# Optimization experiments

Hardware: AMD Instinct MI355X
Metric: run time of the kernel (lower is better)

The kernel has to match this reference:

```python
import jax, jax.numpy as jnp
import numpy as np

N_NODES = 50000
N_EDGES = 800000
N_GRAPHS = 256
IN_DIM = 128
HID = 64
HEADS = 4
N_CLASSES = 2
NEG_SLOPE = 0.2


def gat_conv(h, W, attn_l, attn_r, bias, src, dst, n_heads, out_dim):
    """DGL-style GATConv. h: [N, Fin] -> [N, H, D]."""
    n = h.shape[0]
    feat = (h @ W).reshape(n, n_heads, out_dim)            # [N,H,D]
    el = jnp.sum(feat * attn_l, axis=-1)                   # [N,H]
    er = jnp.sum(feat * attn_r, axis=-1)                   # [N,H]
    e = jax.nn.leaky_relu(el[src] + er[dst], NEG_SLOPE)    # [E,H]
    # edge softmax over incoming edges of each dst node (numerically stable)
    emax = jax.ops.segment_max(e, dst, num_segments=n)     # [N,H]
    emax = jnp.where(jnp.isfinite(emax), emax, 0.0)
    ee = jnp.exp(e - emax[dst])                            # [E,H]
    denom = jax.ops.segment_sum(ee, dst, num_segments=n)   # [N,H]
    alpha = ee / jnp.maximum(denom, 1e-9)[dst]             # [E,H]
    msg = alpha[:, :, None] * feat[src]                    # [E,H,D]
    rst = jax.ops.segment_sum(msg, dst, num_segments=n)    # [N,H,D]
    return rst + bias.reshape(1, n_heads, out_dim)


def setup_inputs() -> dict:
    key = jax.random.key(0)
    ks = jax.random.split(key, 16)
    h = jax.random.normal(ks[0], (N_NODES, IN_DIM), dtype=jnp.float32)
    src = jax.random.randint(ks[1], (N_EDGES,), 0, N_NODES, dtype=jnp.int32)
    dst = jax.random.randint(ks[2], (N_EDGES,), 0, N_NODES, dtype=jnp.int32)
    graph_ids = jnp.sort(jax.random.randint(ks[3], (N_NODES,), 0, N_GRAPHS, dtype=jnp.int32))
    s1 = 1.0 / np.sqrt(IN_DIM)
    s2 = 1.0 / np.sqrt(HID * HEADS)
    sc = 1.0 / np.sqrt(HID)
    W1 = jax.random.normal(ks[4], (IN_DIM, HEADS * HID), dtype=jnp.float32) * s1
    attn_l1 = jax.random.normal(ks[5], (HEADS, HID), dtype=jnp.float32) * sc
    attn_r1 = jax.random.normal(ks[6], (HEADS, HID), dtype=jnp.float32) * sc
    b1 = jnp.zeros((HEADS * HID,), dtype=jnp.float32)
    W2 = jax.random.normal(ks[7], (HEADS * HID, 1 * HID), dtype=jnp.float32) * s2
    attn_l2 = jax.random.normal(ks[8], (1, HID), dtype=jnp.float32) * sc
    attn_r2 = jax.random.normal(ks[9], (1, HID), dtype=jnp.float32) * sc
    b2 = jnp.zeros((HID,), dtype=jnp.float32)
    Wc = jax.random.normal(ks[10], (HID, N_CLASSES), dtype=jnp.float32) * sc
    bc = jnp.zeros((N_CLASSES,), dtype=jnp.float32)
    return {"h": h, "src": src, "dst": dst, "graph_ids": graph_ids,
            "W1": W1, "attn_l1": attn_l1, "attn_r1": attn_r1, "b1": b1,
            "W2": W2, "attn_l2": attn_l2, "attn_r2": attn_r2, "b2": b2,
            "Wc": Wc, "bc": bc}


def reference(h, src, dst, graph_ids, W1, attn_l1, attn_r1, b1,
              W2, attn_l2, attn_r2, b2, Wc, bc):
    # layer 1: [N, IN] -> [N, HEADS, HID] -> relu -> flatten heads
    x = jax.nn.relu(gat_conv(h, W1, attn_l1, attn_r1, b1, src, dst, HEADS, HID))
    x = x.reshape(N_NODES, HEADS * HID)
    # layer 2: single head -> [N, HID]
    x = jax.nn.relu(gat_conv(x, W2, attn_l2, attn_r2, b2, src, dst, 1, HID))
    x = x.reshape(N_NODES, HID)
    # dropout p=0.3 is identity at eval time
    # AvgPooling: mean of node features per graph
    sums = jax.ops.segment_sum(x, graph_ids, num_segments=N_GRAPHS)      # [G,HID]
    cnts = jax.ops.segment_sum(jnp.ones((N_NODES,), x.dtype), graph_ids,
                               num_segments=N_GRAPHS)                    # [G]
    pooled = sums / jnp.maximum(cnts, 1.0)[:, None]
    return pooled @ Wc + bc                                              # [G, n_classes]
```

## Files before the change

kernel.cpp:

```cpp
#include <hip/hip_runtime.h>
#include <math.h>

#define NN 50000
#define NE 800000
#define NG 256
#define IND 128
#define NBUCK 98
#define CHUNK 4096
#define NPBLK ((NE + CHUNK - 1) / CHUNK)

typedef __bf16 bf16_t;
typedef bf16_t bf16x8 __attribute__((ext_vector_type(8)));
typedef float f32x4 __attribute__((ext_vector_type(4)));
typedef float floatx2 __attribute__((ext_vector_type(2)));
typedef unsigned short ushortx8 __attribute__((ext_vector_type(8)));

__device__ __forceinline__ float lrelu(float x) { return fmaxf(x, 0.2f * x); }
__device__ __forceinline__ float b2f(unsigned short u) {
  return __uint_as_float(((unsigned)u) << 16);
}
__device__ __forceinline__ float blo(unsigned u) { return __uint_as_float(u << 16); }
__device__ __forceinline__ float bhi(unsigned u) { return __uint_as_float(u & 0xffff0000u); }
__device__ __forceinline__ unsigned short f2b(float f) {
  unsigned u = __float_as_uint(f);
  return (unsigned short)((u + 0x7fffu + ((u >> 16) & 1u)) >> 16);
}
__device__ __forceinline__ float sel4(float v0, float v1, float v2, float v3, int g) {
  float a01 = (g & 1) ? v1 : v0;
  float a23 = (g & 1) ? v3 : v2;
  return (g & 2) ? a23 : a01;
}

__global__ __launch_bounds__(1024) void k_zero(int* __restrict__ counts) {
  int i = blockIdx.x * 1024 + threadIdx.x;
  if (i < NN) counts[i] = 0;
}

__global__ __launch_bounds__(256) void k_prep(const float* __restrict__ W1,
                                              const int* __restrict__ dst,
                                              unsigned short* __restrict__ w1t_hi,
                                              int* __restrict__ counts) {
  int tid = blockIdx.x * 256 + threadIdx.x;
  if (tid < 256 * IND) {
    int c = tid >> 7, k = tid & 127;
    w1t_hi[tid] = f2b(W1[(size_t)k * 256 + c]);
  }
  if (tid < NE) atomicAdd(&counts[dst[tid]], 1);
}

__global__ __launch_bounds__(256) void k_gemm1(const float* __restrict__ h,
                                               const unsigned short* __restrict__ w1t_hi,
                                               const float* __restrict__ al,
                                               const float* __restrict__ ar,
                                               unsigned int* __restrict__ feat1f8,
                                               float4* __restrict__ el1,
                                               float4* __restrict__ er1) {
  __shared__ unsigned short w1s[256 * IND];
  int t = threadIdx.x;
  for (int i = t; i < 4096; i += 256) {
    int c = i >> 4, k8 = i & 15;
    ushortx8 v = ((const ushortx8*)w1t_hi)[i];
    int byte = (c * 256 + k8 * 16) ^ ((c & 7) << 4);
    *(ushortx8*)((char*)w1s + byte) = v;
  }
  __syncthreads();
  int w = t >> 6, l = t & 63;
  int c0 = l & 15, kg = l >> 4;
  int rw = blockIdx.x * 64 + w * 16;
  int arow = rw + c0;
  if (arow >= NN) arow = NN - 1;
  const float4* hp = (const float4*)h + (size_t)arow * 32 + kg * 2;
  f32x4 acc[16] = {};
#pragma unroll
  for (int ks = 0; ks < 4; ks++) {
    float4 v0 = hp[ks * 8], v1 = hp[ks * 8 + 1];
    float f[8] = {v0.x, v0.y, v0.z, v0.w, v1.x, v1.y, v1.z, v1.w};
    ushortx8 uh, ul;
#pragma unroll
    for (int j = 0; j < 8; j++) {
      unsigned short hj = f2b(f[j]);
      uh[j] = hj;
      ul[j] = f2b(f[j] - b2f(hj));
    }
    bf16x8 ah = *(bf16x8*)&uh;
    bf16x8 alo = *(bf16x8*)&ul;
#pragma unroll
    for (int n = 0; n < 16; n++) {
      int col = n * 16 + c0;
      int byte = (col * 256 + (ks * 4 + kg) * 16) ^ ((col & 7) << 4);
      bf16x8 b = *(const bf16x8*)(const void*)((const char*)w1s + byte);
      acc[n] = __builtin_amdgcn_mfma_f32_16x16x32_bf16(alo, b, acc[n], 0, 0, 0);
      acc[n] = __builtin_amdgcn_mfma_f32_16x16x32_bf16(ah, b, acc[n], 0, 0, 0);
    }
  }
  float alv[16], arv[16];
#pragma unroll
  for (int n = 0; n < 16; n++) {
    int ai = (n >> 2) * 64 + (n & 3) * 16 + c0;
    alv[n] = al[ai];
    arv[n] = ar[ai];
  }
#pragma unroll
  for (int j = 0; j < 4; j++) {
    int node = rw + kg * 4 + j;
    bool ok = node < NN;
    float pl[4] = {0.f, 0.f, 0.f, 0.f}, pr[4] = {0.f, 0.f, 0.f, 0.f};
#pragma unroll
    for (int dq = 0; dq < 4; dq++) {
      float v0 = acc[dq][j], v1 = acc[4 | dq][j], v2 = acc[8 | dq][j], v3 = acc[12 | dq][j];
      if (ok) {
        int u = __builtin_amdgcn_cvt_pk_fp8_f32(v0, v1, 0, false);
        u = __builtin_amdgcn_cvt_pk_fp8_f32(v2, v3, u, true);
        feat1f8[(size_t)node * 64 + dq * 16 + c0] = (unsigned)u;
      }
    }
#pragma unroll
    for (int n = 0; n < 16; n++) {
      float cv = acc[n][j];
      int hh = n >> 2;
      pl[hh] += cv * alv[n];
      pr[hh] += cv * arv[n];
    }
#pragma unroll
    for (int off = 1; off < 16; off <<= 1) {
#pragma unroll
      for (int hh = 0; hh < 4; hh++) {
        pl[hh] += __shfl_xor(pl[hh], off);
        pr[hh] += __shfl_xor(pr[hh], off);
      }
    }
    if (c0 == 0 && ok) {
      el1[node] = make_float4(pl[0], pl[1], pl[2], pl[3]);
      er1[node] = make_float4(pr[0], pr[1], pr[2], pr[3]);
    }
  }
}

#define NSB ((NN + 1023) / 1024)
__global__ __launch_bounds__(1024) void k_scanA(const int* __restrict__ counts,
                                                int* __restrict__ bsums) {
  int gid = blockIdx.x * 1024 + threadIdx.x;
  int v = (gid < NN) ? counts[gid] : 0;
#pragma unroll
  for (int off = 32; off; off >>= 1) v += __shfl_xor(v, off);
  __shared__ int ws[16];
  int w = threadIdx.x >> 6, l = threadIdx.x & 63;
  if (l == 0) ws[w] = v;
  __syncthreads();
  if (threadIdx.x == 0) {
    int s = 0;
#pragma unroll
    for (int i = 0; i < 16; i++) s += ws[i];
    bsums[blockIdx.x] = s;
  }
}

__global__ __launch_bounds__(64) void k_scanB(const int* __restrict__ bsums,
                                              int* __restrict__ boffs,
                                              int* __restrict__ bcursor) {
  int l = threadIdx.x;
  int orig = (l < NSB) ? bsums[l] : 0;
  int v = orig;
#pragma unroll
  for (int off = 1; off < 64; off <<= 1) {
    int tv = __shfl_up(v, off);
    if (l >= off) v += tv;
  }
  if (l < NSB) boffs[l] = v - orig;
  for (int i = l; i < NBUCK; i += 64) bcursor[i] = 0;
}

__global__ __launch_bounds__(1024) void k_scanC(const int* __restrict__ counts,
                                                const int* __restrict__ boffs,
                                                int* __restrict__ offs) {
  int gid = blockIdx.x * 1024 + threadIdx.x;
  int orig = (gid < NN) ? counts[gid] : 0;
  int v = orig;
  int w = threadIdx.x >> 6, l = threadIdx.x & 63;
#pragma unroll
  for (int off = 1; off < 64; off <<= 1) {
    int tv = __shfl_up(v, off);
    if (l >= off) v += tv;
  }
  __shared__ int ws[16];
  if (l == 63) ws[w] = v;
  __syncthreads();
  int woff = 0;
#pragma unroll
  for (int i = 0; i < 16; i++)
    if (i < w) woff += ws[i];
  if (gid < NN) offs[gid] = boffs[blockIdx.x] + woff + v - orig;
  if (gid == 0) offs[NN] = NE;
}

__global__ __launch_bounds__(256) void k_part(const int* __restrict__ src, const int* __restrict__ dst,
                                              const int* __restrict__ offs, int* __restrict__ bcursor,
                                              int2* __restrict__ ebuf) {
  __shared__ int lcnt[NBUCK];
  __shared__ int lbase[NBUCK];
  __shared__ int gb[NBUCK];
  int t = threadIdx.x;
  for (int i = t; i < NBUCK; i += 256) lcnt[i] = 0;
  __syncthreads();
  int e0 = blockIdx.x * CHUNK;
  int sv[16], dv[16], rk[16];
#pragma unroll
  for (int i = 0; i < 16; i++) {
    int e = e0 + i * 256 + t;
    if (e < NE) {
      sv[i] = src[e];
      dv[i] = dst[e];
      rk[i] = atomicAdd(&lcnt[dv[i] >> 9], 1);
    }
  }
  __syncthreads();
  for (int i = t; i < NBUCK; i += 256) {
    lbase[i] = atomicAdd(&bcursor[i], lcnt[i]);
    gb[i] = offs[i << 9];
  }
  __syncthreads();
#pragma unroll
  for (int i = 0; i < 16; i++) {
    int e = e0 + i * 256 + t;
    if (e < NE) {
      int b = dv[i] >> 9;
      int2 v;
      v.x = sv[i];
      v.y = dv[i];
      ebuf[gb[b] + lbase[b] + rk[i]] = v;
    }
  }
}

__global__ __launch_bounds__(256) void k_scat2(const int2* __restrict__ ebuf, const int* __restrict__ offs,
                                               int2* __restrict__ sd) {
  __shared__ int lcur[512];
  int b = blockIdx.x, t = threadIdx.x;
  for (int i = t; i < 512; i += 256) lcur[i] = 0;
  int n0 = b << 9;
  int n1 = n0 + 512;
  if (n1 > NN) n1 = NN;
  int lo = offs[n0], hi = offs[n1];
  __syncthreads();
  for (int i = lo + t; i < hi; i += 256) {
    int2 p = ebuf[i];
    int pos = atomicAdd(&lcur[p.y - n0], 1);
    sd[offs[p.y] + pos] = p;
  }
}

__global__ __launch_bounds__(256) void k_edge1(const int2* __restrict__ sd,
                                               const float4* __restrict__ el1,
                                               const float4* __restrict__ er1,
                                               int4* __restrict__ erec1) {
  int i = blockIdx.x * 256 + threadIdx.x;
  if (i >= NE) return;
  int2 p = sd[i];
  float4 l = el1[p.x], r = er1[p.y];
  unsigned w0 = f2b(__expf(lrelu(l.x + r.x)));
  unsigned w1 = f2b(__expf(lrelu(l.y + r.y)));
  unsigned w2 = f2b(__expf(lrelu(l.z + r.z)));
  unsigned w3 = f2b(__expf(lrelu(l.w + r.w)));
  int4 o;
  o.x = p.x;
  o.y = (int)(w0 | (w1 << 16));
  o.z = (int)(w2 | (w3 << 16));
  o.w = 0;
  erec1[i] = o;
}

__global__ __launch_bounds__(256) void k_agg1(const int* __restrict__ offs, const int4* __restrict__ erec1,
                                              const unsigned int* __restrict__ feat1f8,
                                              const float* __restrict__ b1,
                                              unsigned short* __restrict__ x1b) {
  int wid = (blockIdx.x * 256 + threadIdx.x) >> 6;
  int lane = threadIdx.x & 63;
  if (wid >= NN) return;
  int g = lane >> 4, q = lane & 15;
  int start = offs[wid], end = offs[wid + 1];
  float a[4][4] = {};
  float ds0 = 0.f, ds1 = 0.f, ds2 = 0.f, ds3 = 0.f;
  int i = start;
  for (; i + 8 <= end; i += 8) {
    int4 r0 = erec1[i + g];
    int4 r1 = erec1[i + 4 + g];
    uint4 u0 = *(const uint4*)(feat1f8 + (size_t)r0.x * 64 + q * 4);
    uint4 u1 = *(const uint4*)(feat1f8 + (size_t)r1.x * 64 + q * 4);
    float w00 = blo((unsigned)r0.y), w01 = bhi((unsigned)r0.y);
    float w02 = blo((unsigned)r0.z), w03 = bhi((unsigned)r0.z);
    float w10 = blo((unsigned)r1.y), w11 = bhi((unsigned)r1.y);
    float w12 = blo((unsigned)r1.z), w13 = bhi((unsigned)r1.z);
#pragma unroll
    for (int dj = 0; dj < 4; dj++) {
      unsigned ua = (&u0.x)[dj], ub = (&u1.x)[dj];
      floatx2 lo0 = __builtin_amdgcn_cvt_pk_f32_fp8(ua, false);
      floatx2 hi0 = __builtin_amdgcn_cvt_pk_f32_fp8(ua, true);
      floatx2 lo1 = __builtin_amdgcn_cvt_pk_f32_fp8(ub, false);
      floatx2 hi1 = __builtin_amdgcn_cvt_pk_f32_fp8(ub, true);
      a[dj][0] += w00 * lo0[0] + w10 * lo1[0];
      a[dj][1] += w01 * lo0[1] + w11 * lo1[1];
      a[dj][2] += w02 * hi0[0] + w12 * hi1[0];
      a[dj][3] += w03 * hi0[1] + w13 * hi1[1];
    }
    ds0 += w00 + w10; ds1 += w01 + w11; ds2 += w02 + w12; ds3 += w03 + w13;
  }
  for (; i < end; i += 4) {
    int e = i + g;
    bool valid = e < end;
    int ec = valid ? e : end - 1;
    int4 r0 = erec1[ec];
    float w00 = blo((unsigned)r0.y), w01 = bhi((unsigned)r0.y);
    float w02 = blo((unsigned)r0.z), w03 = bhi((unsigned)r0.z);
    if (!valid) { w00 = 0.f; w01 = 0.f; w02 = 0.f; w03 = 0.f; }
    uint4 u0 = *(const uint4*)(feat1f8 + (size_t)r0.x * 64 + q * 4);
#pragma unroll
    for (int dj = 0; dj < 4; dj++) {
      unsigned ua = (&u0.x)[dj];
      floatx2 lo0 = __builtin_amdgcn_cvt_pk_f32_fp8(ua, false);
      floatx2 hi0 = __builtin_amdgcn_cvt_pk_f32_fp8(ua, true);
      a[dj][0] += w00 * lo0[0];
      a[dj][1] += w01 * lo0[1];
      a[dj][2] += w02 * hi0[0];
      a[dj][3] += w03 * hi0[1];
    }
    ds0 += w00; ds1 += w01; ds2 += w02; ds3 += w03;
  }
#pragma unroll
  for (int off = 16; off < 64; off <<= 1) {
#pragma unroll
    for (int dj = 0; dj < 4; dj++) {
#pragma unroll
      for (int hh = 0; hh < 4; hh++) a[dj][hh] += __shfl_xor(a[dj][hh], off);
    }
    ds0 += __shfl_xor(ds0, off);
    ds1 += __shfl_xor(ds1, off);
    ds2 += __shfl_xor(ds2, off);
    ds3 += __shfl_xor(ds3, off);
  }
  float dsg = sel4(ds0, ds1, ds2, ds3, g);
  float inv = 1.f / fmaxf(dsg, 1e-9f);
  float4 bb = *(const float4*)(b1 + g * 64 + q * 4);
  ushort4 ov;
  ov.x = f2b(fmaxf(sel4(a[0][0], a[0][1], a[0][2], a[0][3], g) * inv + bb.x, 0.f));
  ov.y = f2b(fmaxf(sel4(a[1][0], a[1][1], a[1][2], a[1][3], g) * inv + bb.y, 0.f));
  ov.z = f2b(fmaxf(sel4(a[2][0], a[2][1], a[2][2], a[2][3], g) * inv + bb.z, 0.f));
  ov.w = f2b(fmaxf(sel4(a[3][0], a[3][1], a[3][2], a[3][3], g) * inv + bb.w, 0.f));
  *(ushort4*)(x1b + (size_t)wid * 256 + g * 64 + q * 4) = ov;
}

__global__ __launch_bounds__(256) void k_gemm2(const unsigned short* __restrict__ x1b,
                                               const float* __restrict__ W2,
                                               const float* __restrict__ al2,
                                               const float* __restrict__ ar2,
                                               unsigned int* __restrict__ feat2f8,
                                               float* __restrict__ el2,
                                               float* __restrict__ er2) {
  __shared__ unsigned short w2t[64 * 256];
  int t = threadIdx.x;
  for (int i = t; i < 64 * 256; i += 256) {
    int k = i >> 6, col = i & 63;
    int kg = k >> 3;
    int s = (col * 32 + kg) ^ (col & 7);
    w2t[s * 8 + (k & 7)] = f2b(W2[i]);
  }
  __syncthreads();
  int w = t >> 6, l = t & 63;
  int rw = blockIdx.x * 64 + w * 16;
  int arow = rw + (l & 15);
  if (arow >= NN) arow = NN - 1;
  const unsigned short* aptr = x1b + (size_t)arow * 256 + (l >> 4) * 8;
  f32x4 acc[4] = {};
#pragma unroll
  for (int ks = 0; ks < 8; ks++) {
    bf16x8 a = *(const bf16x8*)(const void*)(aptr + ks * 32);
#pragma unroll
    for (int n = 0; n < 4; n++) {
      int colg = n * 16 + (l & 15);
      int kg = ks * 4 + (l >> 4);
      int s = (colg * 32 + kg) ^ (colg & 7);
      bf16x8 b = *(const bf16x8*)(const void*)&w2t[s * 8];
      acc[n] = __builtin_amdgcn_mfma_f32_16x16x32_bf16(a, b, acc[n], 0, 0, 0);
    }
  }
  float al2v[4], ar2v[4];
#pragma unroll
  for (int n = 0; n < 4; n++) { al2v[n] = al2[n * 16 + (l & 15)]; ar2v[n] = ar2[n * 16 + (l & 15)]; }
#pragma unroll
  for (int j = 0; j < 4; j++) {
    int node = rw + (l >> 4) * 4 + j;
    float pl = 0.f, pr = 0.f;
    float c0v = acc[0][j], c1v = acc[1][j], c2v = acc[2][j], c3v = acc[3][j];
    if (node < NN) {
      int u = __builtin_amdgcn_cvt_pk_fp8_f32(c0v, c1v, 0, false);
      u = __builtin_amdgcn_cvt_pk_fp8_f32(c2v, c3v, u, true);
      feat2f8[(size_t)node * 16 + (l & 15)] = (unsigned)u;
    }
    pl = c0v * al2v[0] + c1v * al2v[1] + c2v * al2v[2] + c3v * al2v[3];
    pr = c0v * ar2v[0] + c1v * ar2v[1] + c2v * ar2v[2] + c3v * ar2v[3];
#pragma unroll
    for (int off = 1; off < 16; off <<= 1) {
      pl += __shfl_xor(pl, off);
      pr += __shfl_xor(pr, off);
    }
    if ((l & 15) == 0 && node < NN) { el2[node] = pl; er2[node] = pr; }
  }
}

__global__ __launch_bounds__(256) void k_edge2(const int2* __restrict__ sd,
                                               const float* __restrict__ el2,
                                               const float* __restrict__ er2,
                                               int2* __restrict__ erec2) {
  int i = blockIdx.x * 256 + threadIdx.x;
  if (i >= NE) return;
  int2 p = sd[i];
  int2 o;
  o.x = p.x;
  o.y = __float_as_int(__expf(lrelu(el2[p.x] + er2[p.y])));
  erec2[i] = o;
}

__global__ __launch_bounds__(256) void k_agg2(const int* __restrict__ offs, const int2* __restrict__ erec2,
                                              const unsigned int* __restrict__ feat2f8,
                                              const float* __restrict__ b2,
                                              unsigned short* __restrict__ x2b) {
  int wid = (blockIdx.x * 256 + threadIdx.x) >> 6;
  int lane = threadIdx.x & 63;
  if (wid >= NN) return;
  int g = lane >> 4, q = lane & 15;
  int start = offs[wid], end = offs[wid + 1];
  float a0 = 0.f, a1 = 0.f, a2 = 0.f, a3 = 0.f, dsum = 0.f;
  int i = start;
  for (; i + 8 <= end; i += 8) {
    int2 r0 = erec2[i + g];
    int2 r1 = erec2[i + 4 + g];
    unsigned u0 = feat2f8[(size_t)r0.x * 16 + q];
    unsigned u1 = feat2f8[(size_t)r1.x * 16 + q];
    float w0 = __int_as_float(r0.y), w1 = __int_as_float(r1.y);
    floatx2 lo0 = __builtin_amdgcn_cvt_pk_f32_fp8(u0, false);
    floatx2 hi0 = __builtin_amdgcn_cvt_pk_f32_fp8(u0, true);
    floatx2 lo1 = __builtin_amdgcn_cvt_pk_f32_fp8(u1, false);
    floatx2 hi1 = __builtin_amdgcn_cvt_pk_f32_fp8(u1, true);
    a0 += w0 * lo0[0] + w1 * lo1[0];
    a1 += w0 * lo0[1] + w1 * lo1[1];
    a2 += w0 * hi0[0] + w1 * hi1[0];
    a3 += w0 * hi0[1] + w1 * hi1[1];
    dsum += w0 + w1;
  }
  for (; i < end; i += 4) {
    int e = i + g;
    bool valid = e < end;
    int ec = valid ? e : end - 1;
    int2 r0 = erec2[ec];
    float w0 = valid ? __int_as_float(r0.y) : 0.f;
    unsigned u0 = feat2f8[(size_t)r0.x * 16 + q];
    floatx2 lo0 = __builtin_amdgcn_cvt_pk_f32_fp8(u0, false);
    floatx2 hi0 = __builtin_amdgcn_cvt_pk_f32_fp8(u0, true);
    a0 += w0 * lo0[0];
    a1 += w0 * lo0[1];
    a2 += w0 * hi0[0];
    a3 += w0 * hi0[1];
    dsum += w0;
  }
#pragma unroll
  for (int off = 16; off < 64; off <<= 1) {
    a0 += __shfl_xor(a0, off);
    a1 += __shfl_xor(a1, off);
    a2 += __shfl_xor(a2, off);
    a3 += __shfl_xor(a3, off);
    dsum += __shfl_xor(dsum, off);
  }
  float inv = 1.f / fmaxf(dsum, 1e-9f);
  float av = sel4(a0, a1, a2, a3, g);
  x2b[(size_t)wid * 64 + lane] = f2b(fmaxf(av * inv + b2[lane], 0.f));
}

__global__ __launch_bounds__(1024) void k_pool(const unsigned short* __restrict__ x2b,
                                               const int* __restrict__ gid,
                                               const float* __restrict__ Wc,
                                               const float* __restrict__ bc,
                                               float* __restrict__ out) {
  int g = blockIdx.x;
  int t = threadIdx.x;
  int lo = 0, hi = NN;
  while (lo < hi) { int mid = (lo + hi) >> 1; if (gid[mid] < g) lo = mid + 1; else hi = mid; }
  int lb = lo;
  hi = NN;
  while (lo < hi) { int mid = (lo + hi) >> 1; if (gid[mid] < g + 1) lo = mid + 1; else hi = mid; }
  int le = lo;
  int d = t & 63, slice = t >> 6;
  float s = 0.f;
  for (int n = lb + slice; n < le; n += 16) s += b2f(x2b[(size_t)n * 64 + d]);
  __shared__ float ws[16][64];
  ws[slice][d] = s;
  __syncthreads();
  if (t < 64) {
    float p = 0.f;
#pragma unroll
    for (int i = 0; i < 16; i++) p += ws[i][d];
    p /= fmaxf((float)(le - lb), 1.f);
    float a0 = p * Wc[d * 2 + 0];
    float a1 = p * Wc[d * 2 + 1];
#pragma unroll
    for (int off = 32; off; off >>= 1) { a0 += __shfl_xor(a0, off); a1 += __shfl_xor(a1, off); }
    if (d == 0) { out[g * 2 + 0] = a0 + bc[0]; out[g * 2 + 1] = a1 + bc[1]; }
  }
}

extern "C" void kernel_launch(void* const* d_in, const int* in_sizes, int n_in,
                              void* d_out, int out_size, void* d_ws, size_t ws_size,
                              hipStream_t stream) {
  const float* h = (const float*)d_in[0];
  const int* src = (const int*)d_in[1];
  const int* dst = (const int*)d_in[2];
  const int* gid = (const int*)d_in[3];
  const float* W1 = (const float*)d_in[4];
  const float* al1 = (const float*)d_in[5];
  const float* ar1 = (const float*)d_in[6];
  const float* b1 = (const float*)d_in[7];
  const float* W2 = (const float*)d_in[8];
  const float* al2 = (const float*)d_in[9];
  const float* ar2 = (const float*)d_in[10];
  const float* b2 = (const float*)d_in[11];
  const float* Wc = (const float*)d_in[12];
  const float* bc = (const float*)d_in[13];
  float* out = (float*)d_out;

  char* wsp = (char*)d_ws;
  size_t off = 0;
  auto take = [&](size_t bytes) -> void* {
    void* p = wsp + off;
    off = (off + bytes + 255) & ~(size_t)255;
    return p;
  };
  unsigned int* feat1f8 = (unsigned int*)take((size_t)NN * 256);
  unsigned short* x1b = (unsigned short*)take((size_t)NN * 256 * 2);
  unsigned int* feat2f8 = (unsigned int*)take((size_t)NN * 64);
  unsigned short* x2b = (unsigned short*)take((size_t)NN * 64 * 2);
  unsigned short* w1t_hi = (unsigned short*)take((size_t)256 * IND * 2);
  float4* el1 = (float4*)take((size_t)NN * 16);
  float4* er1 = (float4*)take((size_t)NN * 16);
  float* el2 = (float*)take((size_t)NN * 4);
  float* er2 = (float*)take((size_t)NN * 4);
  int* counts = (int*)take((size_t)NN * 4);
  int* offs = (int*)take((size_t)(NN + 1) * 4);
  int2* sd = (int2*)take((size_t)NE * 8);
  int2* ebuf = (int2*)take((size_t)NE * 8);
  int4* erec1 = (int4*)take((size_t)NE * 16);
  int2* erec2 = (int2*)take((size_t)NE * 8);
  int* bsums = (int*)take((size_t)NSB * 4);
  int* boffs = (int*)take((size_t)NSB * 4);
  int* bcursor = (int*)take((size_t)NBUCK * 4);

  k_zero<<<NSB, 1024, 0, stream>>>(counts);

  k_prep<<<(NE + 255) / 256, 256, 0, stream>>>(W1, dst, w1t_hi, counts);

  k_scanA<<<NSB, 1024, 0, stream>>>(counts, bsums);
  k_scanB<<<1, 64, 0, stream>>>(bsums, boffs, bcursor);
  k_scanC<<<NSB, 1024, 0, stream>>>(counts, boffs, offs);
  k_part<<<NPBLK, 256, 0, stream>>>(src, dst, offs, bcursor, ebuf);
  k_scat2<<<NBUCK, 256, 0, stream>>>(ebuf, offs, sd);

  k_gemm1<<<(NN + 63) / 64, 256, 0, stream>>>(h, w1t_hi, al1, ar1, feat1f8, el1, er1);
  k_edge1<<<(NE + 255) / 256, 256, 0, stream>>>(sd, el1, er1, erec1);
  k_agg1<<<(NN * 64 + 255) / 256, 256, 0, stream>>>(offs, erec1, feat1f8, b1, x1b);

  k_gemm2<<<(NN + 63) / 64, 256, 0, stream>>>(x1b, W2, al2, ar2, feat2f8, el2, er2);
  k_edge2<<<(NE + 255) / 256, 256, 0, stream>>>(sd, el2, er2, erec2);
  k_agg2<<<(NN * 64 + 255) / 256, 256, 0, stream>>>(offs, erec2, feat2f8, b2, x2b);

  k_pool<<<NG, 1024, 0, stream>>>(x2b, gid, Wc, bc, out);
}
```

Measured before the change: 201.7 us.

## Fuse layer-2 edge weight computation into aggregation, precompute W2 bf16 tile, unroll aggregation loops

Drops the separate k_edge2 kernel and its erec2 buffer. k_agg2 now reads src indices from sd and computes exp(leaky_relu(el2[src]+er2[dst])) inline, with er2 loaded once per destination node. W2 is converted to swizzled bf16 once in k_prep, so each k_gemm2 block does a vector copy into shared memory instead of converting. Both aggregation kernels gain a 16-edge unrolled loop for more memory-level parallelism. This saves a launch and an edge-array round trip, at the cost of extra exp work and gathers in agg2 and higher register pressure from the unrolling.

```diff
diff --git a/kernel.cpp b/kernel.cpp
--- a/kernel.cpp
+++ b/kernel.cpp
@@ -37,13 +37,21 @@
 }
 
 __global__ __launch_bounds__(256) void k_prep(const float* __restrict__ W1,
+                                              const float* __restrict__ W2,
                                               const int* __restrict__ dst,
                                               unsigned short* __restrict__ w1t_hi,
+                                              unsigned short* __restrict__ w2t_pre,
                                               int* __restrict__ counts) {
   int tid = blockIdx.x * 256 + threadIdx.x;
   if (tid < 256 * IND) {
     int c = tid >> 7, k = tid & 127;
     w1t_hi[tid] = f2b(W1[(size_t)k * 256 + c]);
+  } else if (tid < 256 * IND + 64 * 256) {
+    int idx = tid - 256 * IND;
+    int k = idx >> 6, col = idx & 63;
+    int kg = k >> 3;
+    int s = (col * 32 + kg) ^ (col & 7);
+    w2t_pre[s * 8 + (k & 7)] = f2b(W2[idx]);
   }
   if (tid < NE) atomicAdd(&counts[dst[tid]], 1);
 }
@@ -281,6 +289,44 @@
   float a[4][4] = {};
   float ds0 = 0.f, ds1 = 0.f, ds2 = 0.f, ds3 = 0.f;
   int i = start;
+  for (; i + 16 <= end; i += 16) {
+    int4 r0 = erec1[i + g];
+    int4 r1 = erec1[i + 4 + g];
+    int4 r2 = erec1[i + 8 + g];
+    int4 r3 = erec1[i + 12 + g];
+    uint4 u0 = *(const uint4*)(feat1f8 + (size_t)r0.x * 64 + q * 4);
+    uint4 u1 = *(const uint4*)(feat1f8 + (size_t)r1.x * 64 + q * 4);
+    uint4 u2 = *(const uint4*)(feat1f8 + (size_t)r2.x * 64 + q * 4);
+    uint4 u3 = *(const uint4*)(feat1f8 + (size_t)r3.x * 64 + q * 4);
+    float w00 = blo((unsigned)r0.y), w01 = bhi((unsigned)r0.y);
+    float w02 = blo((unsigned)r0.z), w03 = bhi((unsigned)r0.z);
+    float w10 = blo((unsigned)r1.y), w11 = bhi((unsigned)r1.y);
+    float w12 = blo((unsigned)r1.z), w13 = bhi((unsigned)r1.z);
+    float w20 = blo((unsigned)r2.y), w21 = bhi((unsigned)r2.y);
+    float w22 = blo((unsigned)r2.z), w23 = bhi((unsigned)r2.z);
+    float w30 = blo((unsigned)r3.y), w31 = bhi((unsigned)r3.y);
+    float w32 = blo((unsigned)r3.z), w33 = bhi((unsigned)r3.z);
+#pragma unroll
+    for (int dj = 0; dj < 4; dj++) {
+      unsigned ua = (&u0.x)[dj], ub = (&u1.x)[dj], uc = (&u2.x)[dj], ud = (&u3.x)[dj];
+      floatx2 loa = __builtin_amdgcn_cvt_pk_f32_fp8(ua, false);
+      floatx2 hia = __builtin_amdgcn_cvt_pk_f32_fp8(ua, true);
+      floatx2 lob = __builtin_amdgcn_cvt_pk_f32_fp8(ub, false);
+      floatx2 hib = __builtin_amdgcn_cvt_pk_f32_fp8(ub, true);
+      floatx2 loc = __builtin_amdgcn_cvt_pk_f32_fp8(uc, false);
+      floatx2 hic = __builtin_amdgcn_cvt_pk_f32_fp8(uc, true);
+      floatx2 lod = __builtin_amdgcn_cvt_pk_f32_fp8(ud, false);
+      floatx2 hid = __builtin_amdgcn_cvt_pk_f32_fp8(ud, true);
+      a[dj][0] += w00 * loa[0] + w10 * lob[0] + w20 * loc[0] + w30 * lod[0];
+      a[dj][1] += w01 * loa[1] + w11 * lob[1] + w21 * loc[1] + w31 * lod[1];
+      a[dj][2] += w02 * hia[0] + w12 * hib[0] + w22 * hic[0] + w32 * hid[0];
+      a[dj][3] += w03 * hia[1] + w13 * hib[1] + w23 * hic[1] + w33 * hid[1];
+    }
+    ds0 += w00 + w10 + w20 + w30;
+    ds1 += w01 + w11 + w21 + w31;
+    ds2 += w02 + w12 + w22 + w32;
+    ds3 += w03 + w13 + w23 + w33;
+  }
   for (; i + 8 <= end; i += 8) {
     int4 r0 = erec1[i + g];
     int4 r1 = erec1[i + 4 + g];
@@ -349,7 +395,7 @@
 }
 
 __global__ __launch_bounds__(256) void k_gemm2(const unsigned short* __restrict__ x1b,
-                                               const float* __restrict__ W2,
+                                               const unsigned short* __restrict__ w2t_pre,
                                                const float* __restrict__ al2,
                                                const float* __restrict__ ar2,
                                                unsigned int* __restrict__ feat2f8,
@@ -357,12 +403,8 @@
                                                float* __restrict__ er2) {
   __shared__ unsigned short w2t[64 * 256];
   int t = threadIdx.x;
-  for (int i = t; i < 64 * 256; i += 256) {
-    int k = i >> 6, col = i & 63;
-    int kg = k >> 3;
-    int s = (col * 32 + kg) ^ (col & 7);
-    w2t[s * 8 + (k & 7)] = f2b(W2[i]);
-  }
+  for (int i = t; i < 2048; i += 256)
+    ((ushortx8*)w2t)[i] = ((const ushortx8*)w2t_pre)[i];
   __syncthreads();
   int w = t >> 6, l = t & 63;
   int rw = blockIdx.x * 64 + w * 16;
@@ -406,20 +448,8 @@
   }
 }
 
-__global__ __launch_bounds__(256) void k_edge2(const int2* __restrict__ sd,
-                                               const float* __restrict__ el2,
-                                               const float* __restrict__ er2,
-                                               int2* __restrict__ erec2) {
-  int i = blockIdx.x * 256 + threadIdx.x;
-  if (i >= NE) return;
-  int2 p = sd[i];
-  int2 o;
-  o.x = p.x;
-  o.y = __float_as_int(__expf(lrelu(el2[p.x] + er2[p.y])));
-  erec2[i] = o;
-}
-
-__global__ __launch_bounds__(256) void k_agg2(const int* __restrict__ offs, const int2* __restrict__ erec2,
+__global__ __launch_bounds__(256) void k_agg2(const int* __restrict__ offs, const int2* __restrict__ sd,
+                                              const float* __restrict__ el2, const float* __restrict__ er2,
                                               const unsigned int* __restrict__ feat2f8,
                                               const float* __restrict__ b2,
                                               unsigned short* __restrict__ x2b) {
@@ -428,14 +458,39 @@
   if (wid >= NN) return;
   int g = lane >> 4, q = lane & 15;
   int start = offs[wid], end = offs[wid + 1];
+  float erv = er2[wid];
   float a0 = 0.f, a1 = 0.f, a2 = 0.f, a3 = 0.f, dsum = 0.f;
   int i = start;
+  for (; i + 16 <= end; i += 16) {
+    int2 p0 = sd[i + g], p1 = sd[i + 4 + g], p2 = sd[i + 8 + g], p3 = sd[i + 12 + g];
+    unsigned u0 = feat2f8[(size_t)p0.x * 16 + q];
+    unsigned u1 = feat2f8[(size_t)p1.x * 16 + q];
+    unsigned u2 = feat2f8[(size_t)p2.x * 16 + q];
+    unsigned u3 = feat2f8[(size_t)p3.x * 16 + q];
+    float w0 = __expf(lrelu(el2[p0.x] + erv));
+    float w1 = __expf(lrelu(el2[p1.x] + erv));
+    float w2 = __expf(lrelu(el2[p2.x] + erv));
+    float w3 = __expf(lrelu(el2[p3.x] + erv));
+    floatx2 lo0 = __builtin_amdgcn_cvt_pk_f32_fp8(u0, false);
+    floatx2 hi0 = __builtin_amdgcn_cvt_pk_f32_fp8(u0, true);
+    floatx2 lo1 = __builtin_amdgcn_cvt_pk_f32_fp8(u1, false);
+    floatx2 hi1 = __builtin_amdgcn_cvt_pk_f32_fp8(u1, true);
+    floatx2 lo2 = __builtin_amdgcn_cvt_pk_f32_fp8(u2, false);
+    floatx2 hi2 = __builtin_amdgcn_cvt_pk_f32_fp8(u2, true);
+    floatx2 lo3 = __builtin_amdgcn_cvt_pk_f32_fp8(u3, false);
+    floatx2 hi3 = __builtin_amdgcn_cvt_pk_f32_fp8(u3, true);
+    a0 += w0 * lo0[0] + w1 * lo1[0] + w2 * lo2[0] + w3 * lo3[0];
+    a1 += w0 * lo0[1] + w1 * lo1[1] + w2 * lo2[1] + w3 * lo3[1];
+    a2 += w0 * hi0[0] + w1 * hi1[0] + w2 * hi2[0] + w3 * hi3[0];
+    a3 += w0 * hi0[1] + w1 * hi1[1] + w2 * hi2[1] + w3 * hi3[1];
+    dsum += w0 + w1 + w2 + w3;
+  }
   for (; i + 8 <= end; i += 8) {
-    int2 r0 = erec2[i + g];
-    int2 r1 = erec2[i + 4 + g];
-    unsigned u0 = feat2f8[(size_t)r0.x * 16 + q];
-    unsigned u1 = feat2f8[(size_t)r1.x * 16 + q];
-    float w0 = __int_as_float(r0.y), w1 = __int_as_float(r1.y);
+    int2 p0 = sd[i + g], p1 = sd[i + 4 + g];
+    unsigned u0 = feat2f8[(size_t)p0.x * 16 + q];
+    unsigned u1 = feat2f8[(size_t)p1.x * 16 + q];
+    float w0 = __expf(lrelu(el2[p0.x] + erv));
+    float w1 = __expf(lrelu(el2[p1.x] + erv));
     floatx2 lo0 = __builtin_amdgcn_cvt_pk_f32_fp8(u0, false);
     floatx2 hi0 = __builtin_amdgcn_cvt_pk_f32_fp8(u0, true);
     floatx2 lo1 = __builtin_amdgcn_cvt_pk_f32_fp8(u1, false);
@@ -450,9 +505,10 @@
     int e = i + g;
     bool valid = e < end;
     int ec = valid ? e : end - 1;
-    int2 r0 = erec2[ec];
-    float w0 = valid ? __int_as_float(r0.y) : 0.f;
-    unsigned u0 = feat2f8[(size_t)r0.x * 16 + q];
+    int2 p0 = sd[ec];
+    float w0 = __expf(lrelu(el2[p0.x] + erv));
+    if (!valid) w0 = 0.f;
+    unsigned u0 = feat2f8[(size_t)p0.x * 16 + q];
     floatx2 lo0 = __builtin_amdgcn_cvt_pk_f32_fp8(u0, false);
     floatx2 hi0 = __builtin_amdgcn_cvt_pk_f32_fp8(u0, true);
     a0 += w0 * lo0[0];
@@ -537,6 +593,7 @@
   unsigned int* feat2f8 = (unsigned int*)take((size_t)NN * 64);
   unsigned short* x2b = (unsigned short*)take((size_t)NN * 64 * 2);
   unsigned short* w1t_hi = (unsigned short*)take((size_t)256 * IND * 2);
+  unsigned short* w2t_pre = (unsigned short*)take((size_t)64 * 256 * 2);
   float4* el1 = (float4*)take((size_t)NN * 16);
   float4* er1 = (float4*)take((size_t)NN * 16);
   float* el2 = (float*)take((size_t)NN * 4);
@@ -546,14 +603,13 @@
   int2* sd = (int2*)take((size_t)NE * 8);
   int2* ebuf = (int2*)take((size_t)NE * 8);
   int4* erec1 = (int4*)take((size_t)NE * 16);
-  int2* erec2 = (int2*)take((size_t)NE * 8);
   int* bsums = (int*)take((size_t)NSB * 4);
   int* boffs = (int*)take((size_t)NSB * 4);
   int* bcursor = (int*)take((size_t)NBUCK * 4);
 
   k_zero<<<NSB, 1024, 0, stream>>>(counts);
 
-  k_prep<<<(NE + 255) / 256, 256, 0, stream>>>(W1, dst, w1t_hi, counts);
+  k_prep<<<(NE + 255) / 256, 256, 0, stream>>>(W1, W2, dst, w1t_hi, w2t_pre, counts);
 
   k_scanA<<<NSB, 1024, 0, stream>>>(counts, bsums);
   k_scanB<<<1, 64, 0, stream>>>(bsums, boffs, bcursor);
@@ -565,9 +621,8 @@
   k_edge1<<<(NE + 255) / 256, 256, 0, stream>>>(sd, el1, er1, erec1);
   k_agg1<<<(NN * 64 + 255) / 256, 256, 0, stream>>>(offs, erec1, feat1f8, b1, x1b);
 
-  k_gemm2<<<(NN + 63) / 64, 256, 0, stream>>>(x1b, W2, al2, ar2, feat2f8, el2, er2);
-  k_edge2<<<(NE + 255) / 256, 256, 0, stream>>>(sd, el2, er2, erec2);
-  k_agg2<<<(NN * 64 + 255) / 256, 256, 0, stream>>>(offs, erec2, feat2f8, b2, x2b);
+  k_gemm2<<<(NN + 63) / 64, 256, 0, stream>>>(x1b, w2t_pre, al2, ar2, feat2f8, el2, er2);
+  k_agg2<<<(NN * 64 + 255) / 256, 256, 0, stream>>>(offs, sd, el2, er2, feat2f8, b2, x2b);
 
   k_pool<<<NG, 1024, 0, stream>>>(x2b, gid, Wc, bc, out);
 }
```

New measurement: 196.7 us. 2.5% less time.

## Fuse edge-weight kernels into scatter and aggregation; prepack W2 once

Applied to the files above, without the earlier changes.

Computes layer-1 edge attention weights directly inside the CSR scatter kernel, so the separate edge1 pass and the sd array are gone. Layer-2 edge weights are recomputed on the fly inside agg2 from a compact source-index array, which removes edge2 and the erec2 buffer. W2 is converted to swizzled bf16 once in k_prep instead of in every gemm2 block. gemm1 now launches before the scan and partition kernels. The costs are extra exp work and el2 gathers in agg2, and the scat2 kernel, with only 98 blocks, now carries random el1/er1 gathers.

```diff
diff --git a/kernel.cpp b/kernel.cpp
--- a/kernel.cpp
+++ b/kernel.cpp
@@ -37,13 +37,21 @@
 }
 
 __global__ __launch_bounds__(256) void k_prep(const float* __restrict__ W1,
+                                              const float* __restrict__ W2,
                                               const int* __restrict__ dst,
                                               unsigned short* __restrict__ w1t_hi,
+                                              unsigned short* __restrict__ w2t_pre,
                                               int* __restrict__ counts) {
   int tid = blockIdx.x * 256 + threadIdx.x;
   if (tid < 256 * IND) {
     int c = tid >> 7, k = tid & 127;
     w1t_hi[tid] = f2b(W1[(size_t)k * 256 + c]);
+  } else if (tid < 256 * IND + 64 * 256) {
+    int idx = tid - 256 * IND;
+    int k = idx >> 6, col = idx & 63;
+    int kg = k >> 3;
+    int s = (col * 32 + kg) ^ (col & 7);
+    w2t_pre[s * 8 + (k & 7)] = f2b(W2[idx]);
   }
   if (tid < NE) atomicAdd(&counts[dst[tid]], 1);
 }
@@ -233,7 +241,8 @@
 }
 
 __global__ __launch_bounds__(256) void k_scat2(const int2* __restrict__ ebuf, const int* __restrict__ offs,
-                                               int2* __restrict__ sd) {
+                                               const float4* __restrict__ el1, const float4* __restrict__ er1,
+                                               int4* __restrict__ erec1, int* __restrict__ srcs) {
   __shared__ int lcur[512];
   int b = blockIdx.x, t = threadIdx.x;
   for (int i = t; i < 512; i += 256) lcur[i] = 0;
@@ -245,28 +254,20 @@
   for (int i = lo + t; i < hi; i += 256) {
     int2 p = ebuf[i];
     int pos = atomicAdd(&lcur[p.y - n0], 1);
-    sd[offs[p.y] + pos] = p;
-  }
-}
-
-__global__ __launch_bounds__(256) void k_edge1(const int2* __restrict__ sd,
-                                               const float4* __restrict__ el1,
-                                               const float4* __restrict__ er1,
-                                               int4* __restrict__ erec1) {
-  int i = blockIdx.x * 256 + threadIdx.x;
-  if (i >= NE) return;
-  int2 p = sd[i];
-  float4 l = el1[p.x], r = er1[p.y];
-  unsigned w0 = f2b(__expf(lrelu(l.x + r.x)));
-  unsigned w1 = f2b(__expf(lrelu(l.y + r.y)));
-  unsigned w2 = f2b(__expf(lrelu(l.z + r.z)));
-  unsigned w3 = f2b(__expf(lrelu(l.w + r.w)));
-  int4 o;
-  o.x = p.x;
-  o.y = (int)(w0 | (w1 << 16));
-  o.z = (int)(w2 | (w3 << 16));
-  o.w = 0;
-  erec1[i] = o;
+    int slot = offs[p.y] + pos;
+    float4 l = el1[p.x], r = er1[p.y];
+    unsigned w0 = f2b(__expf(lrelu(l.x + r.x)));
+    unsigned w1 = f2b(__expf(lrelu(l.y + r.y)));
+    unsigned w2 = f2b(__expf(lrelu(l.z + r.z)));
+    unsigned w3 = f2b(__expf(lrelu(l.w + r.w)));
+    int4 o;
+    o.x = p.x;
+    o.y = (int)(w0 | (w1 << 16));
+    o.z = (int)(w2 | (w3 << 16));
+    o.w = 0;
+    erec1[slot] = o;
+    srcs[slot] = p.x;
+  }
 }
 
 __global__ __launch_bounds__(256) void k_agg1(const int* __restrict__ offs, const int4* __restrict__ erec1,
@@ -349,7 +350,7 @@
 }
 
 __global__ __launch_bounds__(256) void k_gemm2(const unsigned short* __restrict__ x1b,
-                                               const float* __restrict__ W2,
+                                               const unsigned short* __restrict__ w2t_pre,
                                                const float* __restrict__ al2,
                                                const float* __restrict__ ar2,
                                                unsigned int* __restrict__ feat2f8,
@@ -357,12 +358,8 @@
                                                float* __restrict__ er2) {
   __shared__ unsigned short w2t[64 * 256];
   int t = threadIdx.x;
-  for (int i = t; i < 64 * 256; i += 256) {
-    int k = i >> 6, col = i & 63;
-    int kg = k >> 3;
-    int s = (col * 32 + kg) ^ (col & 7);
-    w2t[s * 8 + (k & 7)] = f2b(W2[i]);
-  }
+  for (int i = t; i < 2048; i += 256)
+    ((ushortx8*)w2t)[i] = ((const ushortx8*)w2t_pre)[i];
   __syncthreads();
   int w = t >> 6, l = t & 63;
   int rw = blockIdx.x * 64 + w * 16;
@@ -406,20 +403,8 @@
   }
 }
 
-__global__ __launch_bounds__(256) void k_edge2(const int2* __restrict__ sd,
-                                               const float* __restrict__ el2,
-                                               const float* __restrict__ er2,
-                                               int2* __restrict__ erec2) {
-  int i = blockIdx.x * 256 + threadIdx.x;
-  if (i >= NE) return;
-  int2 p = sd[i];
-  int2 o;
-  o.x = p.x;
-  o.y = __float_as_int(__expf(lrelu(el2[p.x] + er2[p.y])));
-  erec2[i] = o;
-}
-
-__global__ __launch_bounds__(256) void k_agg2(const int* __restrict__ offs, const int2* __restrict__ erec2,
+__global__ __launch_bounds__(256) void k_agg2(const int* __restrict__ offs, const int* __restrict__ srcs,
+                                              const float* __restrict__ el2, const float* __restrict__ er2,
                                               const unsigned int* __restrict__ feat2f8,
                                               const float* __restrict__ b2,
                                               unsigned short* __restrict__ x2b) {
@@ -428,14 +413,15 @@
   if (wid >= NN) return;
   int g = lane >> 4, q = lane & 15;
   int start = offs[wid], end = offs[wid + 1];
+  float erv = er2[wid];
   float a0 = 0.f, a1 = 0.f, a2 = 0.f, a3 = 0.f, dsum = 0.f;
   int i = start;
   for (; i + 8 <= end; i += 8) {
-    int2 r0 = erec2[i + g];
-    int2 r1 = erec2[i + 4 + g];
-    unsigned u0 = feat2f8[(size_t)r0.x * 16 + q];
-    unsigned u1 = feat2f8[(size_t)r1.x * 16 + q];
-    float w0 = __int_as_float(r0.y), w1 = __int_as_float(r1.y);
+    int s0 = srcs[i + g], s1 = srcs[i + 4 + g];
+    unsigned u0 = feat2f8[(size_t)s0 * 16 + q];
+    unsigned u1 = feat2f8[(size_t)s1 * 16 + q];
+    float w0 = __expf(lrelu(el2[s0] + erv));
+    float w1 = __expf(lrelu(el2[s1] + erv));
     floatx2 lo0 = __builtin_amdgcn_cvt_pk_f32_fp8(u0, false);
     floatx2 hi0 = __builtin_amdgcn_cvt_pk_f32_fp8(u0, true);
     floatx2 lo1 = __builtin_amdgcn_cvt_pk_f32_fp8(u1, false);
@@ -450,9 +436,10 @@
     int e = i + g;
     bool valid = e < end;
     int ec = valid ? e : end - 1;
-    int2 r0 = erec2[ec];
-    float w0 = valid ? __int_as_float(r0.y) : 0.f;
-    unsigned u0 = feat2f8[(size_t)r0.x * 16 + q];
+    int s0 = srcs[ec];
+    float w0 = __expf(lrelu(el2[s0] + erv));
+    if (!valid) w0 = 0.f;
+    unsigned u0 = feat2f8[(size_t)s0 * 16 + q];
     floatx2 lo0 = __builtin_amdgcn_cvt_pk_f32_fp8(u0, false);
     floatx2 hi0 = __builtin_amdgcn_cvt_pk_f32_fp8(u0, true);
     a0 += w0 * lo0[0];
@@ -537,37 +524,36 @@
   unsigned int* feat2f8 = (unsigned int*)take((size_t)NN * 64);
   unsigned short* x2b = (unsigned short*)take((size_t)NN * 64 * 2);
   unsigned short* w1t_hi = (unsigned short*)take((size_t)256 * IND * 2);
+  unsigned short* w2t_pre = (unsigned short*)take((size_t)64 * 256 * 2);
   float4* el1 = (float4*)take((size_t)NN * 16);
   float4* er1 = (float4*)take((size_t)NN * 16);
   float* el2 = (float*)take((size_t)NN * 4);
   float* er2 = (float*)take((size_t)NN * 4);
   int* counts = (int*)take((size_t)NN * 4);
   int* offs = (int*)take((size_t)(NN + 1) * 4);
-  int2* sd = (int2*)take((size_t)NE * 8);
   int2* ebuf = (int2*)take((size_t)NE * 8);
   int4* erec1 = (int4*)take((size_t)NE * 16);
-  int2* erec2 = (int2*)take((size_t)NE * 8);
+  int* srcs = (int*)take((size_t)NE * 4);
   int* bsums = (int*)take((size_t)NSB * 4);
   int* boffs = (int*)take((size_t)NSB * 4);
   int* bcursor = (int*)take((size_t)NBUCK * 4);
 
   k_zero<<<NSB, 1024, 0, stream>>>(counts);
 
-  k_prep<<<(NE + 255) / 256, 256, 0, stream>>>(W1, dst, w1t_hi, counts);
+  k_prep<<<(NE + 255) / 256, 256, 0, stream>>>(W1, W2, dst, w1t_hi, w2t_pre, counts);
+
+  k_gemm1<<<(NN + 63) / 64, 256, 0, stream>>>(h, w1t_hi, al1, ar1, feat1f8, el1, er1);
 
   k_scanA<<<NSB, 1024, 0, stream>>>(counts, bsums);
   k_scanB<<<1, 64, 0, stream>>>(bsums, boffs, bcursor);
   k_scanC<<<NSB, 1024, 0, stream>>>(counts, boffs, offs);
   k_part<<<NPBLK, 256, 0, stream>>>(src, dst, offs, bcursor, ebuf);
-  k_scat2<<<NBUCK, 256, 0, stream>>>(ebuf, offs, sd);
-
-  k_gemm1<<<(NN + 63) / 64, 256, 0, stream>>>(h, w1t_hi, al1, ar1, feat1f8, el1, er1);
-  k_edge1<<<(NE + 255) / 256, 256, 0, stream>>>(sd, el1, er1, erec1);
+  k_scat2<<<NBUCK, 256, 0, stream>>>(ebuf, offs, el1, er1, erec1, srcs);
+
   k_agg1<<<(NN * 64 + 255) / 256, 256, 0, stream>>>(offs, erec1, feat1f8, b1, x1b);
 
-  k_gemm2<<<(NN + 63) / 64, 256, 0, stream>>>(x1b, W2, al2, ar2, feat2f8, el2, er2);
-  k_edge2<<<(NE + 255) / 256, 256, 0, stream>>>(sd, el2, er2, erec2);
-  k_agg2<<<(NN * 64 + 255) / 256, 256, 0, stream>>>(offs, erec2, feat2f8, b2, x2b);
+  k_gemm2<<<(NN + 63) / 64, 256, 0, stream>>>(x1b, w2t_pre, al2, ar2, feat2f8, el2, er2);
+  k_agg2<<<(NN * 64 + 255) / 256, 256, 0, stream>>>(offs, srcs, el2, er2, feat2f8, b2, x2b);
 
   k_pool<<<NG, 1024, 0, stream>>>(x2b, gid, Wc, bc, out);
 }
```

Result: faster. 196.8 us (-2.5%).
